# Optimization experiments

Measured on AMD Instinct MI355X. Metric: run time of the kernel, lower is better.

Reference implementation:

```python
import jax, jax.numpy as jnp
import numpy as np

N = 45056      # 2048 instances * 22 machines
E = 720896     # avg degree 16
FEA = 60       # max_num*6
HID = 256
MACH = 22
NEG_SLOPE = 0.01


def setup_inputs() -> dict:
    key = jax.random.key(0)
    ks = jax.random.split(key, 20)
    x = jax.random.normal(ks[0], (N, FEA), dtype=jnp.float32)
    edge_index = jax.random.randint(ks[1], (2, E), 0, N, dtype=jnp.int64)
    edge_weight = jax.random.uniform(ks[2], (E,), dtype=jnp.float32)

    def lin(k, fan_in, fan_out):
        s = 1.0 / np.sqrt(fan_in)
        kw, kb = jax.random.split(k)
        W = jax.random.uniform(kw, (fan_in, fan_out), minval=-s, maxval=s, dtype=jnp.float32)
        b = jax.random.uniform(kb, (fan_out,), minval=-s, maxval=s, dtype=jnp.float32)
        return W, b

    W1, b1 = lin(ks[3], FEA, HID)
    W2, b2 = lin(ks[4], HID, HID)
    mlp_in = MACH * (HID + FEA)  # 6952
    Wf0, bf0 = lin(ks[5], mlp_in, HID)
    Wf1, bf1 = lin(ks[6], HID, HID)
    Wf2, bf2 = lin(ks[7], HID, HID)
    Wo, bo = lin(ks[8], HID, 4)
    return {"x": x, "edge_index": edge_index, "edge_weight": edge_weight,
            "W1": W1, "b1": b1, "W2": W2, "b2": b2,
            "Wf0": Wf0, "bf0": bf0, "Wf1": Wf1, "bf1": bf1,
            "Wf2": Wf2, "bf2": bf2, "Wo": Wo, "bo": bo}


def _gcn_conv(h, W, b, row, col, norm, n):
    # h' = scatter_add(norm * (hW)[row] -> col) + b   (PyG GCNConv)
    hw = h @ W                                  # [N, out]
    msg = hw[row] * norm[:, None]               # [E+N, out]
    out = jax.ops.segment_sum(msg, col, num_segments=n)
    return out + b


def reference(x, edge_index, edge_weight, W1, b1, W2, b2,
              Wf0, bf0, Wf1, bf1, Wf2, bf2, Wo, bo):
    n = x.shape[0]
    # gcn_norm with self-loops (fill_value=1.0), symmetric normalization
    loop = jnp.arange(n, dtype=edge_index.dtype)
    row = jnp.concatenate([edge_index[0], loop])
    col = jnp.concatenate([edge_index[1], loop])
    ew = jnp.concatenate([edge_weight, jnp.ones((n,), dtype=edge_weight.dtype)])
    deg = jax.ops.segment_sum(ew, col, num_segments=n)
    dinv = jnp.where(deg > 0, jax.lax.rsqrt(jnp.maximum(deg, 1e-12)), 0.0)
    norm = dinv[row] * ew * dinv[col]

    h = _gcn_conv(x, W1, b1, row, col, norm, n)
    h = jax.nn.leaky_relu(h, NEG_SLOPE)
    # dropout p=0.5 is identity in eval mode
    h = _gcn_conv(h, W2, b2, row, col, norm, n)
    h = jax.nn.leaky_relu(h, NEG_SLOPE)

    h = jnp.concatenate([h, x], axis=1)         # [N, HID+FEA]
    flat = h.reshape(n // MACH, -1)             # [B, 22*(HID+FEA)]

    z = jax.nn.leaky_relu(flat @ Wf0 + bf0, NEG_SLOPE)
    z = jax.nn.leaky_relu(z @ Wf1 + bf1, NEG_SLOPE)
    z = jax.nn.leaky_relu(z @ Wf2 + bf2, NEG_SLOPE)
    return z @ Wo + bo                           # [B, 4]
```

## Files before the change

### kernel.cpp

```cpp
#include <hip/hip_runtime.h>
#include <stdint.h>

#define FEA 60
#define HID 256
#define MACH 22
#define PERM 316
#define PERM2 320
#define FLATP2 (MACH * PERM2)
#define NEG 0.01f
#define BCAP 64

typedef __bf16 bf16x8 __attribute__((ext_vector_type(8)));
typedef float f32x4 __attribute__((ext_vector_type(4)));

__device__ __forceinline__ float bf2f(uint16_t u) {
    return __uint_as_float(((uint32_t)u) << 16);
}
__device__ __forceinline__ uint16_t f2bf(float f) {
    uint32_t x = __float_as_uint(f);
    return (uint16_t)((x + 0x7fffu + ((x >> 16) & 1u)) >> 16);
}

__global__ void k_detect_init(const uint32_t* ew_w, const uint32_t* ei_w, int* flags,
                              int* count, int n) {
    int i = blockIdx.x * blockDim.x + threadIdx.x;
    if (i < n) count[i] = 0;
    if (blockIdx.x == 0) {
        __shared__ int c15, onz;
        if (threadIdx.x == 0) { c15 = 0; onz = 0; }
        __syncthreads();
        int a = 0, b = 0;
        for (int k = threadIdx.x; k < 1024; k += 256) {
            if (ew_w[k] & 0x8000u) a++;
            if (ei_w[2 * k + 1] != 0u) b++;
        }
        atomicAdd(&c15, a); atomicAdd(&onz, b);
        __syncthreads();
        if (threadIdx.x == 0) {
            flags[0] = (c15 <= 100) ? 1 : 0;
            flags[1] = (onz < 8) ? 1 : 0;
        }
    }
}

struct Cvt8 {
    const void* src[8];
    float* dst[8];
    long prefix[9];
    int cnt;
};

__global__ void k_cvt_all(const void* xsrc, uint16_t* x64, int n, Cvt8 a, const int* flags) {
    int isbf = flags[0];
    long nx = (long)n * 64;
    long total = nx + a.prefix[a.cnt];
    for (long i = (long)blockIdx.x * blockDim.x + threadIdx.x; i < total;
         i += (long)gridDim.x * blockDim.x) {
        if (i < nx) {
            int col = (int)(i & 63);
            long row = i >> 6;
            uint16_t v = 0;
            if (col < FEA) {
                long s = row * FEA + col;
                v = isbf ? ((const uint16_t*)xsrc)[s] : f2bf(((const float*)xsrc)[s]);
            }
            x64[i] = v;
        } else {
            long ii = i - nx;
            int t = 0;
            while (ii >= a.prefix[t + 1]) t++;
            long j = ii - a.prefix[t];
            a.dst[t][j] = isbf ? bf2f(((const uint16_t*)a.src[t])[j])
                               : ((const float*)a.src[t])[j];
        }
    }
}

struct PrepW {
    const void* wf0; uint16_t* wf0t;
    const void* src3[3]; uint16_t* dst3[3];
    const void* w1; uint16_t* w1t;
};

__global__ __launch_bounds__(256) void k_prep(PrepW a, const int* flags) {
    __shared__ uint16_t s[64][65];
    int isbf = flags[0];
    int b = blockIdx.x;
    int t = threadIdx.x;
    if (b < 440) {
        int g0 = (b >> 2) * 64, n0 = (b & 3) * 64;
#pragma unroll
        for (int i = 0; i < 16; i++) {
            int idx = t + i * 256;
            int gg = idx >> 6, nn = idx & 63;
            int gk = g0 + gg;
            int m = gk / PERM2;
            int k2 = gk - m * PERM2;
            uint16_t v = 0;
            if (k2 < PERM) {
                long off = (long)(m * PERM + k2) * HID + n0 + nn;
                v = isbf ? ((const uint16_t*)a.wf0)[off] : f2bf(((const float*)a.wf0)[off]);
            }
            s[gg][nn] = v;
        }
        __syncthreads();
#pragma unroll
        for (int i = 0; i < 16; i++) {
            int idx = t + i * 256;
            int nn = idx >> 6, gg = idx & 63;
            a.wf0t[(long)(n0 + nn) * FLATP2 + g0 + gg] = s[gg][nn];
        }
    } else if (b < 488) {
        int idx0 = b - 440;
        int z = idx0 >> 4, r = idx0 & 15;
        int k0 = (r >> 2) * 64, n0 = (r & 3) * 64;
        const void* W = a.src3[z];
        uint16_t* Wt = a.dst3[z];
#pragma unroll
        for (int i = 0; i < 16; i++) {
            int idx = t + i * 256;
            int kk = idx >> 6, nn = idx & 63;
            long off = (long)(k0 + kk) * HID + n0 + nn;
            s[kk][nn] = isbf ? ((const uint16_t*)W)[off] : f2bf(((const float*)W)[off]);
        }
        __syncthreads();
#pragma unroll
        for (int i = 0; i < 16; i++) {
            int idx = t + i * 256;
            int nn = idx >> 6, kk = idx & 63;
            Wt[(long)(n0 + nn) * HID + k0 + kk] = s[kk][nn];
        }
    } else {
        int n0 = (b - 488) * 64;
#pragma unroll
        for (int i = 0; i < 16; i++) {
            int idx = t + i * 256;
            int kk = idx >> 6, nn = idx & 63;
            uint16_t v = 0;
            if (kk < FEA) {
                long off = (long)kk * HID + n0 + nn;
                v = isbf ? ((const uint16_t*)a.w1)[off] : f2bf(((const float*)a.w1)[off]);
            }
            s[kk][nn] = v;
        }
        __syncthreads();
#pragma unroll
        for (int i = 0; i < 16; i++) {
            int idx = t + i * 256;
            int nn = idx >> 6, kk = idx & 63;
            a.w1t[(long)(n0 + nn) * 64 + kk] = s[kk][nn];
        }
    }
}

__global__ void k_scatter(const void* ei, const void* ew, int* count, uint2* adj,
                          int E, const int* flags) {
    int e0 = (blockIdx.x * blockDim.x + threadIdx.x) * 2;
    if (e0 >= E) return;
    int i64 = flags[1], isbf = flags[0];
    int r0, r1 = -1, c0, c1 = -1;
    if (i64) {
        const long long* pr = (const long long*)ei + e0;
        const long long* pc = (const long long*)ei + E + e0;
        r0 = (int)pr[0]; c0 = (int)pc[0];
        if (e0 + 1 < E) { r1 = (int)pr[1]; c1 = (int)pc[1]; }
    } else {
        const int* pr = (const int*)ei + e0;
        const int* pc = (const int*)ei + E + e0;
        r0 = pr[0]; c0 = pc[0];
        if (e0 + 1 < E) { r1 = pr[1]; c1 = pc[1]; }
    }
    float w0, w1 = 0.f;
    if (isbf) {
        uint32_t ww = ((const uint32_t*)ew)[e0 >> 1];
        w0 = bf2f((uint16_t)(ww & 0xffff));
        w1 = bf2f((uint16_t)(ww >> 16));
    } else {
        float2 f = ((const float2*)ew)[e0 >> 1];
        w0 = f.x; w1 = f.y;
    }
    int p0 = atomicAdd(&count[c0], 1);
    uint2 v0; v0.x = (uint32_t)r0; v0.y = __float_as_uint(w0);
    adj[((long)c0 << 6) + p0] = v0;
    if (c1 >= 0) {
        int p1 = atomicAdd(&count[c1], 1);
        uint2 v1; v1.x = (uint32_t)r1; v1.y = __float_as_uint(w1);
        adj[((long)c1 << 6) + p1] = v1;
    }
}

__global__ void k_rowsum(const int* count, const uint2* adj, float* dinv, int n) {
    int i = blockIdx.x * blockDim.x + threadIdx.x;
    if (i >= n) return;
    int cnt = count[i];
    const uint2* row = adj + ((long)i << 6);
    double d = 1.0;
    for (int p = 0; p < cnt; p++) d += (double)__uint_as_float(row[p].y);
    dinv[i] = (float)(1.0 / sqrt(d));
}

__global__ __launch_bounds__(256) void k_aggx(const uint16_t* __restrict__ x64,
                                              const float* __restrict__ dinv,
                                              const int* __restrict__ count,
                                              const uint2* __restrict__ adj,
                                              uint16_t* __restrict__ xa, int n) {
    __shared__ uint2 sadj[8][32];
    int hv = threadIdx.x >> 5;
    int l = threadIdx.x & 31;
    int node = blockIdx.x * 8 + hv;
    if (node >= n) return;
    const uint32_t* xu = (const uint32_t*)x64;
    float di = dinv[node];
    float c2 = di * di;
    uint32_t h = xu[(long)node * 32 + l];
    float a0 = c2 * bf2f((uint16_t)(h & 0xffff));
    float a1 = c2 * bf2f((uint16_t)(h >> 16));
    int cnt = count[node];
    const uint2* row = adj + ((long)node << 6);
    for (int base = 0; base < cnt; base += 32) {
        int m = cnt - base; if (m > 32) m = 32;
        if (l < m) {
            uint2 a = row[base + l];
            float w = __uint_as_float(a.y) * dinv[a.x] * di;
            uint2 p; p.x = a.x; p.y = __float_as_uint(w);
            sadj[hv][l] = p;
        }
        int t = 0;
        for (; t + 4 <= m; t += 4) {
            uint2 e0 = sadj[hv][t], e1 = sadj[hv][t + 1], e2 = sadj[hv][t + 2], e3 = sadj[hv][t + 3];
            uint32_t v0 = xu[(long)e0.x * 32 + l];
            uint32_t v1 = xu[(long)e1.x * 32 + l];
            uint32_t v2 = xu[(long)e2.x * 32 + l];
            uint32_t v3 = xu[(long)e3.x * 32 + l];
            float w0 = __uint_as_float(e0.y), w1 = __uint_as_float(e1.y);
            float w2 = __uint_as_float(e2.y), w3 = __uint_as_float(e3.y);
            a0 += w0 * bf2f((uint16_t)(v0 & 0xffff)); a1 += w0 * bf2f((uint16_t)(v0 >> 16));
            a0 += w1 * bf2f((uint16_t)(v1 & 0xffff)); a1 += w1 * bf2f((uint16_t)(v1 >> 16));
            a0 += w2 * bf2f((uint16_t)(v2 & 0xffff)); a1 += w2 * bf2f((uint16_t)(v2 >> 16));
            a0 += w3 * bf2f((uint16_t)(v3 & 0xffff)); a1 += w3 * bf2f((uint16_t)(v3 >> 16));
        }
        for (; t < m; t++) {
            uint2 e0 = sadj[hv][t];
            uint32_t v0 = xu[(long)e0.x * 32 + l];
            float w0 = __uint_as_float(e0.y);
            a0 += w0 * bf2f((uint16_t)(v0 & 0xffff));
            a1 += w0 * bf2f((uint16_t)(v0 >> 16));
        }
    }
    ((uint32_t*)xa)[(long)node * 32 + l] =
        (uint32_t)f2bf(a0) | ((uint32_t)f2bf(a1) << 16);
}

__device__ __forceinline__ void fma8(float* acc, float w, uint4 v) {
    acc[0] += w * bf2f((uint16_t)(v.x & 0xffff));
    acc[1] += w * bf2f((uint16_t)(v.x >> 16));
    acc[2] += w * bf2f((uint16_t)(v.y & 0xffff));
    acc[3] += w * bf2f((uint16_t)(v.y >> 16));
    acc[4] += w * bf2f((uint16_t)(v.z & 0xffff));
    acc[5] += w * bf2f((uint16_t)(v.z >> 16));
    acc[6] += w * bf2f((uint16_t)(v.w & 0xffff));
    acc[7] += w * bf2f((uint16_t)(v.w >> 16));
}

__global__ __launch_bounds__(256) void k_aggb(const uint16_t* __restrict__ hw,
                                              const float* __restrict__ dinv,
                                              const int* __restrict__ count,
                                              const uint2* __restrict__ adj,
                                              const float* __restrict__ bias,
                                              uint16_t* __restrict__ out, int n) {
    __shared__ uint2 sadj[8][32];
    int hv = threadIdx.x >> 5;
    int l = threadIdx.x & 31;
    int node = blockIdx.x * 8 + hv;
    if (node >= n) return;
    const uint4* hw4 = (const uint4*)hw;
    float di = dinv[node];
    float c2 = di * di;
    uint4 h = hw4[(long)node * 32 + l];
    float acc[8];
    acc[0] = c2 * bf2f((uint16_t)(h.x & 0xffff));
    acc[1] = c2 * bf2f((uint16_t)(h.x >> 16));
    acc[2] = c2 * bf2f((uint16_t)(h.y & 0xffff));
    acc[3] = c2 * bf2f((uint16_t)(h.y >> 16));
    acc[4] = c2 * bf2f((uint16_t)(h.z & 0xffff));
    acc[5] = c2 * bf2f((uint16_t)(h.z >> 16));
    acc[6] = c2 * bf2f((uint16_t)(h.w & 0xffff));
    acc[7] = c2 * bf2f((uint16_t)(h.w >> 16));
    int cnt = count[node];
    const uint2* row = adj + ((long)node << 6);
    for (int base = 0; base < cnt; base += 32) {
        int m = cnt - base; if (m > 32) m = 32;
        if (l < m) {
            uint2 a = row[base + l];
            float w = __uint_as_float(a.y) * dinv[a.x] * di;
            uint2 p; p.x = a.x; p.y = __float_as_uint(w);
            sadj[hv][l] = p;
        }
        int t = 0;
        for (; t + 4 <= m; t += 4) {
            uint2 e0 = sadj[hv][t], e1 = sadj[hv][t + 1], e2 = sadj[hv][t + 2], e3 = sadj[hv][t + 3];
            uint4 v0 = hw4[(long)e0.x * 32 + l];
            uint4 v1 = hw4[(long)e1.x * 32 + l];
            uint4 v2 = hw4[(long)e2.x * 32 + l];
            uint4 v3 = hw4[(long)e3.x * 32 + l];
            fma8(acc, __uint_as_float(e0.y), v0);
            fma8(acc, __uint_as_float(e1.y), v1);
            fma8(acc, __uint_as_float(e2.y), v2);
            fma8(acc, __uint_as_float(e3.y), v3);
        }
        for (; t < m; t++) {
            uint2 e0 = sadj[hv][t];
            uint4 v0 = hw4[(long)e0.x * 32 + l];
            fma8(acc, __uint_as_float(e0.y), v0);
        }
    }
    float4 ba = ((const float4*)bias)[l * 2];
    float4 bb = ((const float4*)bias)[l * 2 + 1];
    acc[0] += ba.x; acc[1] += ba.y; acc[2] += ba.z; acc[3] += ba.w;
    acc[4] += bb.x; acc[5] += bb.y; acc[6] += bb.z; acc[7] += bb.w;
#pragma unroll
    for (int k = 0; k < 8; k++) acc[k] = acc[k] > 0.f ? acc[k] : NEG * acc[k];
    uint4 o;
    o.x = (uint32_t)f2bf(acc[0]) | ((uint32_t)f2bf(acc[1]) << 16);
    o.y = (uint32_t)f2bf(acc[2]) | ((uint32_t)f2bf(acc[3]) << 16);
    o.z = (uint32_t)f2bf(acc[4]) | ((uint32_t)f2bf(acc[5]) << 16);
    o.w = (uint32_t)f2bf(acc[6]) | ((uint32_t)f2bf(acc[7]) << 16);
    ((uint4*)out)[(long)node * 32 + l] = o;
}

__global__ __launch_bounds__(256) void k_mgemm(const uint16_t* __restrict__ A,
                                               const uint16_t* __restrict__ Bt,
                                               float* __restrict__ part,
                                               uint16_t* __restrict__ outb,
                                               const float* __restrict__ bias,
                                               int M, int K, int Kc, int act) {
    __shared__ uint16_t As[128 * 40];
    __shared__ uint16_t Bs[128 * 40];
    int tid = threadIdx.x;
    int lane = tid & 63, wv = tid >> 6;
    int quad = lane >> 4, l15 = lane & 15;
    int row0 = blockIdx.y * 128, col0 = blockIdx.x * 128;
    int kbeg = blockIdx.z * Kc;
    int kend = kbeg + Kc; if (kend > K) kend = K;
    int arow = (wv >> 1) * 64;
    int bcol = (wv & 1) * 64;

    f32x4 acc[4][4];
#pragma unroll
    for (int i = 0; i < 4; i++)
#pragma unroll
        for (int j = 0; j < 4; j++) acc[i][j] = (f32x4){0.f, 0.f, 0.f, 0.f};

    for (int kc = kbeg; kc < kend; kc += 32) {
#pragma unroll
        for (int i = 0; i < 2; i++) {
            int idx = tid + i * 256;
            int r = idx >> 2, cq = idx & 3;
            uint4 va = *(const uint4*)(A + (long)(row0 + r) * K + kc + cq * 8);
            *(uint4*)(&As[r * 40 + cq * 8]) = va;
            uint4 vb = *(const uint4*)(Bt + (long)(col0 + r) * K + kc + cq * 8);
            *(uint4*)(&Bs[r * 40 + cq * 8]) = vb;
        }
        __syncthreads();
        bf16x8 af[4], bfr[4];
#pragma unroll
        for (int i = 0; i < 4; i++)
            af[i] = __builtin_bit_cast(bf16x8,
                *(const uint4*)(&As[(arow + i * 16 + l15) * 40 + quad * 8]));
#pragma unroll
        for (int j = 0; j < 4; j++)
            bfr[j] = __builtin_bit_cast(bf16x8,
                *(const uint4*)(&Bs[(bcol + j * 16 + l15) * 40 + quad * 8]));
#pragma unroll
        for (int i = 0; i < 4; i++)
#pragma unroll
            for (int j = 0; j < 4; j++)
                acc[i][j] = __builtin_amdgcn_mfma_f32_16x16x32_bf16(af[i], bfr[j], acc[i][j], 0, 0, 0);
        __syncthreads();
    }

#pragma unroll
    for (int i = 0; i < 4; i++)
#pragma unroll
        for (int j = 0; j < 4; j++) {
            int row = row0 + arow + i * 16 + quad * 4;
            int col = col0 + bcol + j * 16 + l15;
#pragma unroll
            for (int reg = 0; reg < 4; reg++) {
                float v = acc[i][j][reg];
                long o = (long)(row + reg) * HID + col;
                if (part) part[(long)blockIdx.z * M * HID + o] = v;
                else {
                    if (bias) v += bias[col];
                    if (act) v = v > 0.f ? v : NEG * v;
                    outb[o] = f2bf(v);
                }
            }
        }
}

__global__ __launch_bounds__(256) void k_mgemm_flat(const uint16_t* __restrict__ h2,
                                                    const uint16_t* __restrict__ x64,
                                                    const uint16_t* __restrict__ Bt,
                                                    float* __restrict__ part,
                                                    int M, int Kc) {
    __shared__ uint16_t As[128 * 40];
    __shared__ uint16_t Bs[128 * 40];
    int tid = threadIdx.x;
    int lane = tid & 63, wv = tid >> 6;
    int quad = lane >> 4, l15 = lane & 15;
    int row0 = blockIdx.y * 128, col0 = blockIdx.x * 128;
    int kbeg = blockIdx.z * Kc;
    int kend = kbeg + Kc; if (kend > FLATP2) kend = FLATP2;
    int arow = (wv >> 1) * 64;
    int bcol = (wv & 1) * 64;

    f32x4 acc[4][4];
#pragma unroll
    for (int i = 0; i < 4; i++)
#pragma unroll
        for (int j = 0; j < 4; j++) acc[i][j] = (f32x4){0.f, 0.f, 0.f, 0.f};

    for (int kc = kbeg; kc < kend; kc += 32) {
#pragma unroll
        for (int i = 0; i < 2; i++) {
            int idx = tid + i * 256;
            int r = idx >> 2, cq = idx & 3;
            int gk = kc + cq * 8;
            int m = gk / PERM2;
            int k2 = gk - m * PERM2;
            long node = (long)(row0 + r) * MACH + m;
            uint4 va = (k2 < HID)
                ? *(const uint4*)(h2 + node * HID + k2)
                : *(const uint4*)(x64 + node * 64 + (k2 - HID));
            *(uint4*)(&As[r * 40 + cq * 8]) = va;
            uint4 vb = *(const uint4*)(Bt + (long)(col0 + r) * FLATP2 + gk);
            *(uint4*)(&Bs[r * 40 + cq * 8]) = vb;
        }
        __syncthreads();
        bf16x8 af[4], bfr[4];
#pragma unroll
        for (int i = 0; i < 4; i++)
            af[i] = __builtin_bit_cast(bf16x8,
                *(const uint4*)(&As[(arow + i * 16 + l15) * 40 + quad * 8]));
#pragma unroll
        for (int j = 0; j < 4; j++)
            bfr[j] = __builtin_bit_cast(bf16x8,
                *(const uint4*)(&Bs[(bcol + j * 16 + l15) * 40 + quad * 8]));
#pragma unroll
        for (int i = 0; i < 4; i++)
#pragma unroll
            for (int j = 0; j < 4; j++)
                acc[i][j] = __builtin_amdgcn_mfma_f32_16x16x32_bf16(af[i], bfr[j], acc[i][j], 0, 0, 0);
        __syncthreads();
    }

#pragma unroll
    for (int i = 0; i < 4; i++)
#pragma unroll
        for (int j = 0; j < 4; j++) {
            int row = row0 + arow + i * 16 + quad * 4;
            int col = col0 + bcol + j * 16 + l15;
#pragma unroll
            for (int reg = 0; reg < 4; reg++)
                part[(long)blockIdx.z * M * HID + (long)(row + reg) * HID + col] = acc[i][j][reg];
        }
}

#define S0 8
__global__ __launch_bounds__(256) void k_tail(const float* __restrict__ part,
                                              const float* __restrict__ bf0,
                                              const uint16_t* __restrict__ Wf1t,
                                              const float* __restrict__ bf1,
                                              const uint16_t* __restrict__ Wf2t,
                                              const float* __restrict__ bf2,
                                              const float* __restrict__ Wo,
                                              const float* __restrict__ bo,
                                              void* out, const int* flags, int MN) {
    __shared__ uint16_t z0s[16 * 256];
    __shared__ uint16_t z1s[16 * 256];
    __shared__ uint16_t z2s[16 * 256];
    int tid = threadIdx.x;
    int lane = tid & 63, wv = tid >> 6;
    int quad = lane >> 4, l15 = lane & 15;
    int rows0 = blockIdx.x * 16;
    int nw = wv * 64;

    for (int i = tid; i < 16 * 256; i += 256) {
        int rr = i >> 8, cc = i & 255;
        long idx = (long)(rows0 + rr) * HID + cc;
        float v = 0.f;
#pragma unroll
        for (int s = 0; s < S0; s++) v += part[(long)s * MN + idx];
        v += bf0[cc];
        v = v > 0.f ? v : NEG * v;
        z0s[i] = f2bf(v);
    }
    __syncthreads();

    {
        f32x4 acc[4];
#pragma unroll
        for (int j = 0; j < 4; j++) acc[j] = (f32x4){0.f, 0.f, 0.f, 0.f};
        for (int kc = 0; kc < HID; kc += 32) {
            bf16x8 a = __builtin_bit_cast(bf16x8,
                *(const uint4*)(&z0s[l15 * 256 + kc + quad * 8]));
#pragma unroll
            for (int j = 0; j < 4; j++) {
                bf16x8 b = __builtin_bit_cast(bf16x8,
                    *(const uint4*)(Wf1t + (long)(nw + j * 16 + l15) * HID + kc + quad * 8));
                acc[j] = __builtin_amdgcn_mfma_f32_16x16x32_bf16(a, b, acc[j], 0, 0, 0);
            }
        }
#pragma unroll
        for (int j = 0; j < 4; j++) {
            int col = nw + j * 16 + l15;
            float bj = bf1[col];
#pragma unroll
            for (int reg = 0; reg < 4; reg++) {
                float v = acc[j][reg] + bj;
                v = v > 0.f ? v : NEG * v;
                z1s[(quad * 4 + reg) * 256 + col] = f2bf(v);
            }
        }
    }
    __syncthreads();

    {
        f32x4 acc[4];
#pragma unroll
        for (int j = 0; j < 4; j++) acc[j] = (f32x4){0.f, 0.f, 0.f, 0.f};
        for (int kc = 0; kc < HID; kc += 32) {
            bf16x8 a = __builtin_bit_cast(bf16x8,
                *(const uint4*)(&z1s[l15 * 256 + kc + quad * 8]));
#pragma unroll
            for (int j = 0; j < 4; j++) {
                bf16x8 b = __builtin_bit_cast(bf16x8,
                    *(const uint4*)(Wf2t + (long)(nw + j * 16 + l15) * HID + kc + quad * 8));
                acc[j] = __builtin_amdgcn_mfma_f32_16x16x32_bf16(a, b, acc[j], 0, 0, 0);
            }
        }
#pragma unroll
        for (int j = 0; j < 4; j++) {
            int col = nw + j * 16 + l15;
            float bj = bf2[col];
#pragma unroll
            for (int reg = 0; reg < 4; reg++) {
                float v = acc[j][reg] + bj;
                v = v > 0.f ? v : NEG * v;
                z2s[(quad * 4 + reg) * 256 + col] = f2bf(v);
            }
        }
    }
    __syncthreads();

    if (tid < 64) {
        int r = tid >> 2, o = tid & 3;
        float acc = bo[o];
        for (int k = 0; k < HID; k++)
            acc += bf2f(z2s[r * 256 + k]) * Wo[k * 4 + o];
        long idx = (long)(rows0 + r) * 4 + o;
        if (flags[0]) ((uint16_t*)out)[idx] = f2bf(acc);
        else          ((float*)out)[idx] = acc;
    }
}

extern "C" void kernel_launch(void* const* d_in, const int* in_sizes, int n_in,
                              void* d_out, int out_size, void* d_ws, size_t ws_size,
                              hipStream_t stream) {
    const int N  = in_sizes[0] / FEA;
    const int E  = in_sizes[2];
    const int Bn = N / MACH;
    const int Kc0 = 896;

    char* ws = (char*)d_ws;
    size_t off = 0;
    auto alloc = [&](size_t bytes) -> char* {
        char* p = ws + off;
        off = (off + bytes + 255) & ~(size_t)255;
        return p;
    };

    int*      flags  = (int*)     alloc(64);
    uint16_t* x64    = (uint16_t*)alloc((size_t)N * 64 * 2);
    uint16_t* xa     = (uint16_t*)alloc((size_t)N * 64 * 2);
    uint16_t* W1t    = (uint16_t*)alloc((size_t)HID * 64 * 2);
    uint16_t* W2t    = (uint16_t*)alloc((size_t)HID * HID * 2);
    uint16_t* Wf0t   = (uint16_t*)alloc((size_t)HID * FLATP2 * 2);
    uint16_t* Wf1t   = (uint16_t*)alloc((size_t)HID * HID * 2);
    uint16_t* Wf2t   = (uint16_t*)alloc((size_t)HID * HID * 2);
    float*    b1     = (float*)   alloc(HID * 4);
    float*    b2     = (float*)   alloc(HID * 4);
    float*    bf0    = (float*)   alloc(HID * 4);
    float*    bf1    = (float*)   alloc(HID * 4);
    float*    bf2    = (float*)   alloc(HID * 4);
    float*    Wo     = (float*)   alloc((size_t)HID * 4 * 4);
    float*    bo     = (float*)   alloc(4 * 4);
    int*      count  = (int*)     alloc((size_t)N * 4);
    uint2*    adj    = (uint2*)   alloc((size_t)N * BCAP * 8);
    float*    dinv   = (float*)   alloc((size_t)N * 4);
    uint16_t* P      = (uint16_t*)alloc((size_t)N * HID * 2);
    uint16_t* Q      = (uint16_t*)alloc((size_t)N * HID * 2);
    float*    part   = (float*)   alloc((size_t)S0 * Bn * HID * 4);
    (void)ws_size; (void)n_in; (void)out_size;

    k_detect_init<<<(N + 255) / 256, 256, 0, stream>>>(
        (const uint32_t*)d_in[2], (const uint32_t*)d_in[1], flags, count, N);

    Cvt8 c8{};
    const void* s8[7] = { d_in[4], d_in[6], d_in[8], d_in[10], d_in[12], d_in[13], d_in[14] };
    float* d8[7] = { b1, b2, bf0, bf1, bf2, Wo, bo };
    long n8[7] = { HID, HID, HID, HID, HID, (long)HID * 4, 4 };
    c8.cnt = 7;
    c8.prefix[0] = 0;
    for (int t = 0; t < 7; t++) { c8.src[t] = s8[t]; c8.dst[t] = d8[t]; c8.prefix[t + 1] = c8.prefix[t] + n8[t]; }
    c8.prefix[8] = c8.prefix[7];
    k_cvt_all<<<2048, 256, 0, stream>>>(d_in[0], x64, N, c8, flags);
    PrepW pw{};
    pw.wf0 = d_in[7]; pw.wf0t = Wf0t;
    pw.src3[0] = d_in[5];  pw.dst3[0] = W2t;
    pw.src3[1] = d_in[9];  pw.dst3[1] = Wf1t;
    pw.src3[2] = d_in[11]; pw.dst3[2] = Wf2t;
    pw.w1 = d_in[3]; pw.w1t = W1t;
    k_prep<<<492, 256, 0, stream>>>(pw, flags);

    k_scatter<<<(E / 2 + 255) / 256, 256, 0, stream>>>(d_in[1], d_in[2], count, adj, E, flags);
    k_rowsum<<<(N + 255) / 256, 256, 0, stream>>>(count, adj, dinv, N);

    k_aggx<<<(N + 7) / 8, 256, 0, stream>>>(x64, dinv, count, adj, xa, N);
    k_mgemm<<<dim3(2, N / 128, 1), 256, 0, stream>>>(xa, W1t, nullptr, P, b1, N, 64, 64, 1);

    k_mgemm<<<dim3(2, N / 128, 1), 256, 0, stream>>>(P, W2t, nullptr, Q, nullptr, N, HID, HID, 0);
    k_aggb<<<(N + 7) / 8, 256, 0, stream>>>(Q, dinv, count, adj, b2, P, N);

    k_mgemm_flat<<<dim3(2, Bn / 128, S0), 256, 0, stream>>>(P, x64, Wf0t, part, Bn, Kc0);

    k_tail<<<Bn / 16, 256, 0, stream>>>(part, bf0, Wf1t, bf1, Wf2t, bf2, Wo, bo,
                                        d_out, flags, Bn * HID);
}
```

Before: 321.7 us.

## Merge prep kernels into one launch and use atomic split-K for the flat GEMM

Combines input conversion, weight transposes and edge scatter into a single kernel, dispatched by block-index ranges, to cut launch count and let the independent work run concurrently. The first MLP GEMM doubles its split-K factor (16 slices of 448) and accumulates into one fp32 buffer with atomicAdd, replacing the 8-way partial-sum buffer that the tail kernel had to read and reduce. The accumulator is zeroed in the init kernel, whose grid is enlarged to cover it. The trade-off is about 8M float atomics, with their contention cost, and a non-deterministic summation order.

```diff
diff --git a/kernel.cpp b/kernel.cpp
--- a/kernel.cpp
+++ b/kernel.cpp
@@ -9,6 +9,8 @@
 #define FLATP2 (MACH * PERM2)
 #define NEG 0.01f
 #define BCAP 64
+#define S0 16
+#define KC0 448
 
 typedef __bf16 bf16x8 __attribute__((ext_vector_type(8)));
 typedef float f32x4 __attribute__((ext_vector_type(4)));
@@ -22,9 +24,10 @@
 }
 
 __global__ void k_detect_init(const uint32_t* ew_w, const uint32_t* ei_w, int* flags,
-                              int* count, int n) {
+                              int* count, float* z0acc, int n) {
     int i = blockIdx.x * blockDim.x + threadIdx.x;
     if (i < n) count[i] = 0;
+    z0acc[i] = 0.f;
     if (blockIdx.x == 0) {
         __shared__ int c15, onz;
         if (threadIdx.x == 0) { c15 = 0; onz = 0; }
@@ -43,149 +46,146 @@
     }
 }
 
-struct Cvt8 {
-    const void* src[8];
-    float* dst[8];
-    long prefix[9];
-    int cnt;
-};
-
-__global__ void k_cvt_all(const void* xsrc, uint16_t* x64, int n, Cvt8 a, const int* flags) {
-    int isbf = flags[0];
-    long nx = (long)n * 64;
-    long total = nx + a.prefix[a.cnt];
-    for (long i = (long)blockIdx.x * blockDim.x + threadIdx.x; i < total;
-         i += (long)gridDim.x * blockDim.x) {
-        if (i < nx) {
-            int col = (int)(i & 63);
-            long row = i >> 6;
-            uint16_t v = 0;
-            if (col < FEA) {
-                long s = row * FEA + col;
-                v = isbf ? ((const uint16_t*)xsrc)[s] : f2bf(((const float*)xsrc)[s]);
-            }
-            x64[i] = v;
-        } else {
-            long ii = i - nx;
-            int t = 0;
-            while (ii >= a.prefix[t + 1]) t++;
-            long j = ii - a.prefix[t];
-            a.dst[t][j] = isbf ? bf2f(((const uint16_t*)a.src[t])[j])
-                               : ((const float*)a.src[t])[j];
-        }
-    }
-}
-
-struct PrepW {
+struct PrepAll {
+    const void* xsrc; uint16_t* x64;
+    const void* src8[8]; float* dst8[8]; long prefix[9]; int cnt8;
     const void* wf0; uint16_t* wf0t;
     const void* src3[3]; uint16_t* dst3[3];
     const void* w1; uint16_t* w1t;
+    const void* ei; const void* ew; int* count; uint2* adj; int E;
+    int n;
 };
 
-__global__ __launch_bounds__(256) void k_prep(PrepW a, const int* flags) {
-    __shared__ uint16_t s[64][65];
+#define NB_CVT 1024
+#define NB_TR  492
+
+__global__ __launch_bounds__(256) void k_prep_all(PrepAll a, const int* flags) {
     int isbf = flags[0];
     int b = blockIdx.x;
     int t = threadIdx.x;
-    if (b < 440) {
-        int g0 = (b >> 2) * 64, n0 = (b & 3) * 64;
-#pragma unroll
-        for (int i = 0; i < 16; i++) {
-            int idx = t + i * 256;
-            int gg = idx >> 6, nn = idx & 63;
-            int gk = g0 + gg;
-            int m = gk / PERM2;
-            int k2 = gk - m * PERM2;
-            uint16_t v = 0;
-            if (k2 < PERM) {
-                long off = (long)(m * PERM + k2) * HID + n0 + nn;
-                v = isbf ? ((const uint16_t*)a.wf0)[off] : f2bf(((const float*)a.wf0)[off]);
-            }
-            s[gg][nn] = v;
-        }
-        __syncthreads();
-#pragma unroll
-        for (int i = 0; i < 16; i++) {
-            int idx = t + i * 256;
-            int nn = idx >> 6, gg = idx & 63;
-            a.wf0t[(long)(n0 + nn) * FLATP2 + g0 + gg] = s[gg][nn];
-        }
-    } else if (b < 488) {
-        int idx0 = b - 440;
-        int z = idx0 >> 4, r = idx0 & 15;
-        int k0 = (r >> 2) * 64, n0 = (r & 3) * 64;
-        const void* W = a.src3[z];
-        uint16_t* Wt = a.dst3[z];
-#pragma unroll
-        for (int i = 0; i < 16; i++) {
-            int idx = t + i * 256;
-            int kk = idx >> 6, nn = idx & 63;
-            long off = (long)(k0 + kk) * HID + n0 + nn;
-            s[kk][nn] = isbf ? ((const uint16_t*)W)[off] : f2bf(((const float*)W)[off]);
-        }
-        __syncthreads();
-#pragma unroll
-        for (int i = 0; i < 16; i++) {
-            int idx = t + i * 256;
-            int nn = idx >> 6, kk = idx & 63;
-            Wt[(long)(n0 + nn) * HID + k0 + kk] = s[kk][nn];
+    if (b < NB_CVT) {
+        long nx = (long)a.n * 64;
+        long total = nx + a.prefix[a.cnt8];
+        for (long i = (long)b * 256 + t; i < total; i += (long)NB_CVT * 256) {
+            if (i < nx) {
+                int col = (int)(i & 63);
+                long row = i >> 6;
+                uint16_t v = 0;
+                if (col < FEA) {
+                    long s = row * FEA + col;
+                    v = isbf ? ((const uint16_t*)a.xsrc)[s] : f2bf(((const float*)a.xsrc)[s]);
+                }
+                a.x64[i] = v;
+            } else {
+                long ii = i - nx;
+                int tt = 0;
+                while (ii >= a.prefix[tt + 1]) tt++;
+                long j = ii - a.prefix[tt];
+                a.dst8[tt][j] = isbf ? bf2f(((const uint16_t*)a.src8[tt])[j])
+                                     : ((const float*)a.src8[tt])[j];
+            }
+        }
+    } else if (b < NB_CVT + NB_TR) {
+        __shared__ uint16_t s[64][65];
+        int bb = b - NB_CVT;
+        if (bb < 440) {
+            int g0 = (bb >> 2) * 64, n0 = (bb & 3) * 64;
+#pragma unroll
+            for (int i = 0; i < 16; i++) {
+                int idx = t + i * 256;
+                int gg = idx >> 6, nn = idx & 63;
+                int gk = g0 + gg;
+                int m = gk / PERM2;
+                int k2 = gk - m * PERM2;
+                uint16_t v = 0;
+                if (k2 < PERM) {
+                    long off = (long)(m * PERM + k2) * HID + n0 + nn;
+                    v = isbf ? ((const uint16_t*)a.wf0)[off] : f2bf(((const float*)a.wf0)[off]);
+                }
+                s[gg][nn] = v;
+            }
+            __syncthreads();
+#pragma unroll
+            for (int i = 0; i < 16; i++) {
+                int idx = t + i * 256;
+                int nn = idx >> 6, gg = idx & 63;
+                a.wf0t[(long)(n0 + nn) * FLATP2 + g0 + gg] = s[gg][nn];
+            }
+        } else if (bb < 488) {
+            int idx0 = bb - 440;
+            int z = idx0 >> 4, r = idx0 & 15;
+            int k0 = (r >> 2) * 64, n0 = (r & 3) * 64;
+            const void* W = a.src3[z];
+            uint16_t* Wt = a.dst3[z];
+#pragma unroll
+            for (int i = 0; i < 16; i++) {
+                int idx = t + i * 256;
+                int kk = idx >> 6, nn = idx & 63;
+                long off = (long)(k0 + kk) * HID + n0 + nn;
+                s[kk][nn] = isbf ? ((const uint16_t*)W)[off] : f2bf(((const float*)W)[off]);
+            }
+            __syncthreads();
+#pragma unroll
+            for (int i = 0; i < 16; i++) {
+                int idx = t + i * 256;
+                int nn = idx >> 6, kk = idx & 63;
+                Wt[(long)(n0 + nn) * HID + k0 + kk] = s[kk][nn];
+            }
+        } else {
+            int n0 = (bb - 488) * 64;
+#pragma unroll
+            for (int i = 0; i < 16; i++) {
+                int idx = t + i * 256;
+                int kk = idx >> 6, nn = idx & 63;
+                uint16_t v = 0;
+                if (kk < FEA) {
+                    long off = (long)kk * HID + n0 + nn;
+                    v = isbf ? ((const uint16_t*)a.w1)[off] : f2bf(((const float*)a.w1)[off]);
+                }
+                s[kk][nn] = v;
+            }
+            __syncthreads();
+#pragma unroll
+            for (int i = 0; i < 16; i++) {
+                int idx = t + i * 256;
+                int nn = idx >> 6, kk = idx & 63;
+                a.w1t[(long)(n0 + nn) * 64 + kk] = s[kk][nn];
+            }
         }
     } else {
-        int n0 = (b - 488) * 64;
-#pragma unroll
-        for (int i = 0; i < 16; i++) {
-            int idx = t + i * 256;
-            int kk = idx >> 6, nn = idx & 63;
-            uint16_t v = 0;
-            if (kk < FEA) {
-                long off = (long)kk * HID + n0 + nn;
-                v = isbf ? ((const uint16_t*)a.w1)[off] : f2bf(((const float*)a.w1)[off]);
-            }
-            s[kk][nn] = v;
-        }
-        __syncthreads();
-#pragma unroll
-        for (int i = 0; i < 16; i++) {
-            int idx = t + i * 256;
-            int nn = idx >> 6, kk = idx & 63;
-            a.w1t[(long)(n0 + nn) * 64 + kk] = s[kk][nn];
-        }
-    }
-}
-
-__global__ void k_scatter(const void* ei, const void* ew, int* count, uint2* adj,
-                          int E, const int* flags) {
-    int e0 = (blockIdx.x * blockDim.x + threadIdx.x) * 2;
-    if (e0 >= E) return;
-    int i64 = flags[1], isbf = flags[0];
-    int r0, r1 = -1, c0, c1 = -1;
-    if (i64) {
-        const long long* pr = (const long long*)ei + e0;
-        const long long* pc = (const long long*)ei + E + e0;
-        r0 = (int)pr[0]; c0 = (int)pc[0];
-        if (e0 + 1 < E) { r1 = (int)pr[1]; c1 = (int)pc[1]; }
-    } else {
-        const int* pr = (const int*)ei + e0;
-        const int* pc = (const int*)ei + E + e0;
-        r0 = pr[0]; c0 = pc[0];
-        if (e0 + 1 < E) { r1 = pr[1]; c1 = pc[1]; }
-    }
-    float w0, w1 = 0.f;
-    if (isbf) {
-        uint32_t ww = ((const uint32_t*)ew)[e0 >> 1];
-        w0 = bf2f((uint16_t)(ww & 0xffff));
-        w1 = bf2f((uint16_t)(ww >> 16));
-    } else {
-        float2 f = ((const float2*)ew)[e0 >> 1];
-        w0 = f.x; w1 = f.y;
-    }
-    int p0 = atomicAdd(&count[c0], 1);
-    uint2 v0; v0.x = (uint32_t)r0; v0.y = __float_as_uint(w0);
-    adj[((long)c0 << 6) + p0] = v0;
-    if (c1 >= 0) {
-        int p1 = atomicAdd(&count[c1], 1);
-        uint2 v1; v1.x = (uint32_t)r1; v1.y = __float_as_uint(w1);
-        adj[((long)c1 << 6) + p1] = v1;
+        int e0 = ((b - NB_CVT - NB_TR) * 256 + t) * 2;
+        int E = a.E;
+        if (e0 >= E) return;
+        int i64 = flags[1];
+        int r0, r1 = -1, c0, c1 = -1;
+        if (i64) {
+            const long long* pr = (const long long*)a.ei + e0;
+            const long long* pc = (const long long*)a.ei + E + e0;
+            r0 = (int)pr[0]; c0 = (int)pc[0];
+            if (e0 + 1 < E) { r1 = (int)pr[1]; c1 = (int)pc[1]; }
+        } else {
+            const int* pr = (const int*)a.ei + e0;
+            const int* pc = (const int*)a.ei + E + e0;
+            r0 = pr[0]; c0 = pc[0];
+            if (e0 + 1 < E) { r1 = pr[1]; c1 = pc[1]; }
+        }
+        float w0, w1 = 0.f;
+        if (isbf) {
+            uint32_t ww = ((const uint32_t*)a.ew)[e0 >> 1];
+            w0 = bf2f((uint16_t)(ww & 0xffff));
+            w1 = bf2f((uint16_t)(ww >> 16));
+        } else {
+            float2 f = ((const float2*)a.ew)[e0 >> 1];
+            w0 = f.x; w1 = f.y;
+        }
+        int p0 = atomicAdd(&a.count[c0], 1);
+        uint2 v0; v0.x = (uint32_t)r0; v0.y = __float_as_uint(w0);
+        a.adj[((long)c0 << 6) + p0] = v0;
+        if (c1 >= 0) {
+            int p1 = atomicAdd(&a.count[c1], 1);
+            uint2 v1; v1.x = (uint32_t)r1; v1.y = __float_as_uint(w1);
+            a.adj[((long)c1 << 6) + p1] = v1;
+        }
     }
 }
 
@@ -330,18 +330,15 @@
 
 __global__ __launch_bounds__(256) void k_mgemm(const uint16_t* __restrict__ A,
                                                const uint16_t* __restrict__ Bt,
-                                               float* __restrict__ part,
                                                uint16_t* __restrict__ outb,
                                                const float* __restrict__ bias,
-                                               int M, int K, int Kc, int act) {
+                                               int M, int K, int act) {
     __shared__ uint16_t As[128 * 40];
     __shared__ uint16_t Bs[128 * 40];
     int tid = threadIdx.x;
     int lane = tid & 63, wv = tid >> 6;
     int quad = lane >> 4, l15 = lane & 15;
     int row0 = blockIdx.y * 128, col0 = blockIdx.x * 128;
-    int kbeg = blockIdx.z * Kc;
-    int kend = kbeg + Kc; if (kend > K) kend = K;
     int arow = (wv >> 1) * 64;
     int bcol = (wv & 1) * 64;
 
@@ -351,7 +348,7 @@
 #pragma unroll
         for (int j = 0; j < 4; j++) acc[i][j] = (f32x4){0.f, 0.f, 0.f, 0.f};
 
-    for (int kc = kbeg; kc < kend; kc += 32) {
+    for (int kc = 0; kc < K; kc += 32) {
 #pragma unroll
         for (int i = 0; i < 2; i++) {
             int idx = tid + i * 256;
@@ -388,13 +385,9 @@
 #pragma unroll
             for (int reg = 0; reg < 4; reg++) {
                 float v = acc[i][j][reg];
-                long o = (long)(row + reg) * HID + col;
-                if (part) part[(long)blockIdx.z * M * HID + o] = v;
-                else {
-                    if (bias) v += bias[col];
-                    if (act) v = v > 0.f ? v : NEG * v;
-                    outb[o] = f2bf(v);
-                }
+                if (bias) v += bias[col];
+                if (act) v = v > 0.f ? v : NEG * v;
+                outb[(long)(row + reg) * HID + col] = f2bf(v);
             }
         }
 }
@@ -402,16 +395,16 @@
 __global__ __launch_bounds__(256) void k_mgemm_flat(const uint16_t* __restrict__ h2,
                                                     const uint16_t* __restrict__ x64,
                                                     const uint16_t* __restrict__ Bt,
-                                                    float* __restrict__ part,
-                                                    int M, int Kc) {
+                                                    float* __restrict__ z0acc,
+                                                    int M) {
     __shared__ uint16_t As[128 * 40];
     __shared__ uint16_t Bs[128 * 40];
     int tid = threadIdx.x;
     int lane = tid & 63, wv = tid >> 6;
     int quad = lane >> 4, l15 = lane & 15;
     int row0 = blockIdx.y * 128, col0 = blockIdx.x * 128;
-    int kbeg = blockIdx.z * Kc;
-    int kend = kbeg + Kc; if (kend > FLATP2) kend = FLATP2;
+    int kbeg = blockIdx.z * KC0;
+    int kend = kbeg + KC0; if (kend > FLATP2) kend = FLATP2;
     int arow = (wv >> 1) * 64;
     int bcol = (wv & 1) * 64;
 
@@ -463,12 +456,11 @@
             int col = col0 + bcol + j * 16 + l15;
 #pragma unroll
             for (int reg = 0; reg < 4; reg++)
-                part[(long)blockIdx.z * M * HID + (long)(row + reg) * HID + col] = acc[i][j][reg];
-        }
-}
-
-#define S0 8
-__global__ __launch_bounds__(256) void k_tail(const float* __restrict__ part,
+                atomicAdd(&z0acc[(long)(row + reg) * HID + col], acc[i][j][reg]);
+        }
+}
+
+__global__ __launch_bounds__(256) void k_tail(const float* __restrict__ z0acc,
                                               const float* __restrict__ bf0,
                                               const uint16_t* __restrict__ Wf1t,
                                               const float* __restrict__ bf1,
@@ -476,7 +468,7 @@
                                               const float* __restrict__ bf2,
                                               const float* __restrict__ Wo,
                                               const float* __restrict__ bo,
-                                              void* out, const int* flags, int MN) {
+                                              void* out, const int* flags) {
     __shared__ uint16_t z0s[16 * 256];
     __shared__ uint16_t z1s[16 * 256];
     __shared__ uint16_t z2s[16 * 256];
@@ -488,11 +480,7 @@
 
     for (int i = tid; i < 16 * 256; i += 256) {
         int rr = i >> 8, cc = i & 255;
-        long idx = (long)(rows0 + rr) * HID + cc;
-        float v = 0.f;
-#pragma unroll
-        for (int s = 0; s < S0; s++) v += part[(long)s * MN + idx];
-        v += bf0[cc];
+        float v = z0acc[(long)(rows0 + rr) * HID + cc] + bf0[cc];
         v = v > 0.f ? v : NEG * v;
         z0s[i] = f2bf(v);
     }
@@ -571,7 +559,6 @@
     const int N  = in_sizes[0] / FEA;
     const int E  = in_sizes[2];
     const int Bn = N / MACH;
-    const int Kc0 = 896;
 
     char* ws = (char*)d_ws;
     size_t off = 0;
@@ -601,40 +588,41 @@
     float*    dinv   = (float*)   alloc((size_t)N * 4);
     uint16_t* P      = (uint16_t*)alloc((size_t)N * HID * 2);
     uint16_t* Q      = (uint16_t*)alloc((size_t)N * HID * 2);
-    float*    part   = (float*)   alloc((size_t)S0 * Bn * HID * 4);
+    float*    z0acc  = (float*)   alloc((size_t)Bn * HID * 4);
     (void)ws_size; (void)n_in; (void)out_size;
 
-    k_detect_init<<<(N + 255) / 256, 256, 0, stream>>>(
-        (const uint32_t*)d_in[2], (const uint32_t*)d_in[1], flags, count, N);
-
-    Cvt8 c8{};
+    k_detect_init<<<(Bn * HID) / 256, 256, 0, stream>>>(
+        (const uint32_t*)d_in[2], (const uint32_t*)d_in[1], flags, count, z0acc, N);
+
+    PrepAll pa{};
+    pa.xsrc = d_in[0]; pa.x64 = x64;
     const void* s8[7] = { d_in[4], d_in[6], d_in[8], d_in[10], d_in[12], d_in[13], d_in[14] };
     float* d8[7] = { b1, b2, bf0, bf1, bf2, Wo, bo };
     long n8[7] = { HID, HID, HID, HID, HID, (long)HID * 4, 4 };
-    c8.cnt = 7;
-    c8.prefix[0] = 0;
-    for (int t = 0; t < 7; t++) { c8.src[t] = s8[t]; c8.dst[t] = d8[t]; c8.prefix[t + 1] = c8.prefix[t] + n8[t]; }
-    c8.prefix[8] = c8.prefix[7];
-    k_cvt_all<<<2048, 256, 0, stream>>>(d_in[0], x64, N, c8, flags);
-    PrepW pw{};
-    pw.wf0 = d_in[7]; pw.wf0t = Wf0t;
-    pw.src3[0] = d_in[5];  pw.dst3[0] = W2t;
-    pw.src3[1] = d_in[9];  pw.dst3[1] = Wf1t;
-    pw.src3[2] = d_in[11]; pw.dst3[2] = Wf2t;
-    pw.w1 = d_in[3]; pw.w1t = W1t;
-    k_prep<<<492, 256, 0, stream>>>(pw, flags);
-
-    k_scatter<<<(E / 2 + 255) / 256, 256, 0, stream>>>(d_in[1], d_in[2], count, adj, E, flags);
+    pa.cnt8 = 7;
+    pa.prefix[0] = 0;
+    for (int t = 0; t < 7; t++) { pa.src8[t] = s8[t]; pa.dst8[t] = d8[t]; pa.prefix[t + 1] = pa.prefix[t] + n8[t]; }
+    pa.prefix[8] = pa.prefix[7];
+    pa.wf0 = d_in[7]; pa.wf0t = Wf0t;
+    pa.src3[0] = d_in[5];  pa.dst3[0] = W2t;
+    pa.src3[1] = d_in[9];  pa.dst3[1] = Wf1t;
+    pa.src3[2] = d_in[11]; pa.dst3[2] = Wf2t;
+    pa.w1 = d_in[3]; pa.w1t = W1t;
+    pa.ei = d_in[1]; pa.ew = d_in[2]; pa.count = count; pa.adj = adj; pa.E = E;
+    pa.n = N;
+    int nb_sc = (E / 2 + 255) / 256;
+    k_prep_all<<<NB_CVT + NB_TR + nb_sc, 256, 0, stream>>>(pa, flags);
+
     k_rowsum<<<(N + 255) / 256, 256, 0, stream>>>(count, adj, dinv, N);
 
     k_aggx<<<(N + 7) / 8, 256, 0, stream>>>(x64, dinv, count, adj, xa, N);
-    k_mgemm<<<dim3(2, N / 128, 1), 256, 0, stream>>>(xa, W1t, nullptr, P, b1, N, 64, 64, 1);
-
-    k_mgemm<<<dim3(2, N / 128, 1), 256, 0, stream>>>(P, W2t, nullptr, Q, nullptr, N, HID, HID, 0);
+    k_mgemm<<<dim3(2, N / 128), 256, 0, stream>>>(xa, W1t, P, b1, N, 64, 1);
+
+    k_mgemm<<<dim3(2, N / 128), 256, 0, stream>>>(P, W2t, Q, nullptr, N, HID, 0);
     k_aggb<<<(N + 7) / 8, 256, 0, stream>>>(Q, dinv, count, adj, b2, P, N);
 
-    k_mgemm_flat<<<dim3(2, Bn / 128, S0), 256, 0, stream>>>(P, x64, Wf0t, part, Bn, Kc0);
-
-    k_tail<<<Bn / 16, 256, 0, stream>>>(part, bf0, Wf1t, bf1, Wf2t, bf2, Wo, bo,
-                                        d_out, flags, Bn * HID);
-}
+    k_mgemm_flat<<<dim3(2, Bn / 128, S0), 256, 0, stream>>>(P, x64, Wf0t, z0acc, Bn);
+
+    k_tail<<<Bn / 16, 256, 0, stream>>>(z0acc, bf0, Wf1t, bf1, Wf2t, bf2, Wo, bo,
+                                        d_out, flags);
+}
```

After: 317.2 us. About the same (-1.4%).
